# Optimization experiments

Hardware: AMD Instinct MI355X
Metric: run time of the kernel (lower is better)

Reference implementation:

```python
import jax, jax.numpy as jnp
import numpy as np

B = 16
CLS_OUT = 80
SCORE_THR = 0.05
IOU_THR = 0.65
MAX_NUM = 100
# FPN levels for a 1280x1280 input: (H, W, stride)
LEVELS = [(160, 160, 8), (80, 80, 16), (40, 40, 32)]
N = sum(h * w for h, w, _ in LEVELS)  # 33600


def make_priors():
    # mmdet MlvlPointGenerator(with_stride=True, offset=0): [x*stride, y*stride, stride, stride]
    ps = []
    for h, w, s in LEVELS:
        ys, xs = np.meshgrid(np.arange(h, dtype=np.float32), np.arange(w, dtype=np.float32), indexing='ij')
        st = np.full((h, w), float(s), dtype=np.float32)
        ps.append(np.stack([xs * s, ys * s, st, st], -1).reshape(-1, 4))
    return jnp.asarray(np.concatenate(ps, 0))


def setup_inputs() -> dict:
    key = jax.random.key(0)
    k1, k2, k3 = jax.random.split(key, 3)
    return {
        'cls_scores': jax.random.normal(k1, (B, N, CLS_OUT), dtype=jnp.float32),
        'bbox_preds': jax.random.normal(k2, (B, N, 4), dtype=jnp.float32),
        'objectness': jax.random.normal(k3, (B, N), dtype=jnp.float32),
        'priors': make_priors(),  # [N, 4]
    }


def _bbox_decode(priors, bbox_preds):
    # xy = pred_xy * stride + center;  wh = exp(pred_wh) * stride
    xys = bbox_preds[..., :2] * priors[:, 2:] + priors[:, :2]
    whs = jnp.exp(bbox_preds[..., 2:]) * priors[:, 2:]
    tl = xys - whs * 0.5
    br = xys + whs * 0.5
    return jnp.concatenate([tl, br], axis=-1)  # [B, N, 4] as (x1, y1, x2, y2)


def _iou_matrix(b1, b2):
    # b1: [M,4], b2: [M,4] -> [M,M], matching torch_cal_bbox_ious (no +1 offsets, eps=1e-8)
    x1 = jnp.maximum(b1[:, None, 0], b2[None, :, 0])
    y1 = jnp.maximum(b1[:, None, 1], b2[None, :, 1])
    x2 = jnp.minimum(b1[:, None, 2], b2[None, :, 2])
    y2 = jnp.minimum(b1[:, None, 3], b2[None, :, 3])
    inter = jnp.clip(x2 - x1, 0.0) * jnp.clip(y2 - y1, 0.0)
    a1 = (b1[:, 2] - b1[:, 0]) * (b1[:, 3] - b1[:, 1])
    a2 = (b2[:, 2] - b2[:, 0]) * (b2[:, 3] - b2[:, 1])
    union = a1[:, None] + a2[None, :] - inter
    return inter / (union + 1e-8)


def _nms_single(boxes, scores, labels, valid):
    # Take top MAX_NUM by score (invalid -> -inf), then class-aware greedy suppression.
    masked = jnp.where(valid, scores, -jnp.inf)
    order = jnp.argsort(-masked)[:MAX_NUM]
    b = boxes[order]          # [M,4]
    s = scores[order]         # [M]
    l = labels[order]         # [M]
    v = valid[order]          # [M]
    iou = _iou_matrix(b, b)
    same = l[:, None] == l[None, :]
    idx = jnp.arange(MAX_NUM)

    def body(i, keep):
        sup = keep[i] & same[i] & (iou[i] >= IOU_THR) & (idx > i)
        return keep & ~sup

    keep = jax.lax.fori_loop(0, MAX_NUM, body, v)
    dets = jnp.where(keep[:, None], jnp.concatenate([b, s[:, None]], -1), 0.0)  # [M,5]
    labs = jnp.where(keep, l, -1)
    return dets, labs, keep


def reference(cls_scores, bbox_preds, objectness, priors):
    cls = jax.nn.sigmoid(cls_scores)                  # [B,N,C]
    obj = jax.nn.sigmoid(objectness)                  # [B,N]
    bboxes = _bbox_decode(priors, bbox_preds)         # [B,N,4]
    max_scores = jnp.max(cls, axis=-1)                # [B,N]
    labels = jnp.argmax(cls, axis=-1).astype(jnp.int32)
    scores = max_scores * obj
    valid = scores >= SCORE_THR
    dets, labs, keep = jax.vmap(_nms_single)(bboxes, scores, labels, valid)
    out = jnp.concatenate([dets, labs[..., None].astype(jnp.float32)], -1)  # [B,MAX_NUM,6]
    return out, keep
```

## Files before the change

kernel.cpp:

```cpp
#include <hip/hip_runtime.h>
#include <cstddef>
#include <cstdint>

#define BB 16
#define NN 33600
#define CC 80
#define MAXN 100
#define NBINS 4096
#define MAXC 1024
#define SCORE_THR_F 0.05f
#define IOU_THR_F 0.65f

#define NCHUNK 525
#define K1_CPB 4
#define K1_GX ((NCHUNK + K1_CPB - 1) / K1_CPB)
#define K2T 512

__global__ __launch_bounds__(256) void k1_score(const float* __restrict__ cls,
                                                const float* __restrict__ obj,
                                                float* __restrict__ masked) {
  const int b = blockIdx.y;
  const int q = threadIdx.x & 3;
  const int r = threadIdx.x >> 2;
  const int c_end = min(blockIdx.x * K1_CPB + K1_CPB, NCHUNK);
  for (int c = blockIdx.x * K1_CPB; c < c_end; c++) {
    const int n = c * 64 + r;
    const float4* row = (const float4*)(cls + ((size_t)b * NN + n) * CC);
    float m = -INFINITY;
#pragma unroll
    for (int j = 0; j < 5; j++) {
      float4 v = row[q + 4 * j];
      m = fmaxf(m, fmaxf(fmaxf(v.x, v.y), fmaxf(v.z, v.w)));
    }
#pragma unroll
    for (int d = 1; d < 4; d <<= 1) m = fmaxf(m, __shfl_xor(m, d, 4));
    if (q == 0) {
      float o = obj[(size_t)b * NN + n];
      float s = (1.0f / (1.0f + expf(-m))) * (1.0f / (1.0f + expf(-o)));
      masked[(size_t)b * NN + n] = (s >= SCORE_THR_F) ? s : -INFINITY;
    }
  }
}

__device__ __forceinline__ int score_bin(float s) {
  return min(NBINS - 1, (int)(s * (float)NBINS));
}

__global__ __launch_bounds__(K2T) void k2_all(const float* __restrict__ cls,
                                              const float* __restrict__ bbox,
                                              const float* __restrict__ priors,
                                              const float* __restrict__ masked,
                                              float* __restrict__ out) {
  const int b = blockIdx.x;
  const int tid = threadIdx.x;

  __shared__ int hist[NBINS];
  __shared__ int sfx[K2T];
  __shared__ int s_t, s_cnt;
  __shared__ float cs[MAXC];
  __shared__ int ci[MAXC];
  __shared__ int sel[MAXN];
  __shared__ float sb[MAXN][4];
  __shared__ float ssc[MAXN];
  __shared__ int slab[MAXN];
  __shared__ unsigned int sup[MAXN][4];
  __shared__ unsigned int keepw[4];

  const float4* msc4 = (const float4*)(masked + (size_t)b * NN);

  for (int i = tid; i < NBINS; i += K2T) hist[i] = 0;
  if (tid == 0) { s_t = 0; s_cnt = 0; }
  __syncthreads();

  for (int i = tid; i < NN / 4; i += K2T) {
    float4 v = msc4[i];
    if (v.x >= SCORE_THR_F) atomicAdd(&hist[score_bin(v.x)], 1);
    if (v.y >= SCORE_THR_F) atomicAdd(&hist[score_bin(v.y)], 1);
    if (v.z >= SCORE_THR_F) atomicAdd(&hist[score_bin(v.z)], 1);
    if (v.w >= SCORE_THR_F) atomicAdd(&hist[score_bin(v.w)], 1);
  }
  __syncthreads();

  int sum = 0;
#pragma unroll
  for (int j = 0; j < NBINS / K2T; j++) sum += hist[tid * (NBINS / K2T) + j];
  sfx[tid] = sum;
  __syncthreads();
  for (int off = 1; off < K2T; off <<= 1) {
    int v = sfx[tid];
    int add = (tid + off < K2T) ? sfx[tid + off] : 0;
    __syncthreads();
    sfx[tid] = v + add;
    __syncthreads();
  }
  {
    int Sc = sfx[tid];
    int Sn = (tid < K2T - 1) ? sfx[tid + 1] : 0;
    if (Sc >= MAXN && Sn < MAXN) {
      int running = Sn;
      const int lo = tid * (NBINS / K2T);
      for (int bin = lo + (NBINS / K2T) - 1; bin >= lo; bin--) {
        running += hist[bin];
        if (running >= MAXN) { s_t = bin; break; }
      }
    }
  }
  __syncthreads();
  const int t = s_t;

  for (int i = tid; i < NN / 4; i += K2T) {
    float4 v = msc4[i];
    int base = i * 4;
    if (v.x >= SCORE_THR_F && score_bin(v.x) >= t) {
      int p = atomicAdd(&s_cnt, 1); if (p < MAXC) { cs[p] = v.x; ci[p] = base; }
    }
    if (v.y >= SCORE_THR_F && score_bin(v.y) >= t) {
      int p = atomicAdd(&s_cnt, 1); if (p < MAXC) { cs[p] = v.y; ci[p] = base + 1; }
    }
    if (v.z >= SCORE_THR_F && score_bin(v.z) >= t) {
      int p = atomicAdd(&s_cnt, 1); if (p < MAXC) { cs[p] = v.z; ci[p] = base + 2; }
    }
    if (v.w >= SCORE_THR_F && score_bin(v.w) >= t) {
      int p = atomicAdd(&s_cnt, 1); if (p < MAXC) { cs[p] = v.w; ci[p] = base + 3; }
    }
  }
  __syncthreads();
  const int C = min(s_cnt, MAXC);

  for (int k = tid; k < MAXN; k += K2T) sel[k] = -1;
  __syncthreads();

  for (int i = tid; i < C; i += K2T) {
    float si = cs[i]; int ii = ci[i];
    int r = 0;
    for (int j = 0; j < C; j++) {
      float sj = cs[j]; int ij = ci[j];
      r += (sj > si) || (sj == si && ij < ii);
    }
    if (r < MAXN) { sel[r] = ii; ssc[r] = si; }
  }
  __syncthreads();

  if (tid < MAXN) {
    int idx = sel[tid];
    if (idx >= 0) {
      float4 p = ((const float4*)priors)[idx];
      float4 d = ((const float4*)bbox)[(size_t)b * NN + idx];
      float cx = d.x * p.z + p.x;
      float cy = d.y * p.w + p.y;
      float hw = expf(d.z) * p.z * 0.5f;
      float hh = expf(d.w) * p.w * 0.5f;
      sb[tid][0] = cx - hw; sb[tid][1] = cy - hh;
      sb[tid][2] = cx + hw; sb[tid][3] = cy + hh;
      const float4* crow = (const float4*)(cls + ((size_t)b * NN + idx) * CC);
      float m = -INFINITY; int lab = 0;
#pragma unroll 4
      for (int j = 0; j < CC / 4; j++) {
        float4 v = crow[j];
        int c0 = 4 * j;
        if (v.x > m) { m = v.x; lab = c0; }
        if (v.y > m) { m = v.y; lab = c0 + 1; }
        if (v.z > m) { m = v.z; lab = c0 + 2; }
        if (v.w > m) { m = v.w; lab = c0 + 3; }
      }
      slab[tid] = lab;
    } else {
      sb[tid][0] = 0.f; sb[tid][1] = 0.f; sb[tid][2] = 0.f; sb[tid][3] = 0.f;
      ssc[tid] = 0.f; slab[tid] = -1;
    }
  }
  for (int i = tid; i < MAXN * 4; i += K2T) ((unsigned int*)sup)[i] = 0;
  __syncthreads();

  for (int p = tid; p < MAXN * MAXN; p += K2T) {
    int i = p / MAXN, j = p % MAXN;
    if (j > i && sel[i] >= 0 && sel[j] >= 0 && slab[i] == slab[j]) {
      float xx1 = fmaxf(sb[i][0], sb[j][0]);
      float yy1 = fmaxf(sb[i][1], sb[j][1]);
      float xx2 = fminf(sb[i][2], sb[j][2]);
      float yy2 = fminf(sb[i][3], sb[j][3]);
      float inter = fmaxf(xx2 - xx1, 0.f) * fmaxf(yy2 - yy1, 0.f);
      float ai = (sb[i][2] - sb[i][0]) * (sb[i][3] - sb[i][1]);
      float aj = (sb[j][2] - sb[j][0]) * (sb[j][3] - sb[j][1]);
      float iou = inter / (ai + aj - inter + 1e-8f);
      if (iou >= IOU_THR_F) atomicOr(&sup[i][j >> 5], 1u << (j & 31));
    }
  }
  __syncthreads();

  if (tid == 0) {
    unsigned int kw0 = 0, kw1 = 0, kw2 = 0, kw3 = 0;
    for (int k = 0; k < MAXN; k++)
      if (sel[k] >= 0) {
        if (k < 32) kw0 |= 1u << k;
        else if (k < 64) kw1 |= 1u << (k - 32);
        else if (k < 96) kw2 |= 1u << (k - 64);
        else kw3 |= 1u << (k - 96);
      }
    for (int i = 0; i < MAXN; i++) {
      unsigned int bit = (i < 32) ? (kw0 >> i) : (i < 64) ? (kw1 >> (i - 32))
                        : (i < 96) ? (kw2 >> (i - 64)) : (kw3 >> (i - 96));
      if (bit & 1u) {
        kw0 &= ~sup[i][0]; kw1 &= ~sup[i][1];
        kw2 &= ~sup[i][2]; kw3 &= ~sup[i][3];
      }
    }
    keepw[0] = kw0; keepw[1] = kw1; keepw[2] = kw2; keepw[3] = kw3;
  }
  __syncthreads();

  if (tid < MAXN) {
    int k = tid;
    bool kp = (keepw[k >> 5] >> (k & 31)) & 1u;
    float* row = out + ((size_t)b * MAXN + k) * 6;
    if (kp) {
      row[0] = sb[k][0]; row[1] = sb[k][1]; row[2] = sb[k][2]; row[3] = sb[k][3];
      row[4] = ssc[k];   row[5] = (float)slab[k];
    } else {
      row[0] = 0.f; row[1] = 0.f; row[2] = 0.f; row[3] = 0.f;
      row[4] = 0.f; row[5] = -1.f;
    }
    out[(size_t)BB * MAXN * 6 + (size_t)b * MAXN + k] = kp ? 1.0f : 0.0f;
  }
}

extern "C" void kernel_launch(void* const* d_in, const int* in_sizes, int n_in,
                              void* d_out, int out_size, void* d_ws, size_t ws_size,
                              hipStream_t stream) {
  const float* cls    = (const float*)d_in[0];
  const float* bbox   = (const float*)d_in[1];
  const float* obj    = (const float*)d_in[2];
  const float* priors = (const float*)d_in[3];
  float* out = (float*)d_out;
  float* masked = (float*)d_ws;

  k1_score<<<dim3(K1_GX, BB), 256, 0, stream>>>(cls, obj, masked);
  k2_all<<<BB, K2T, 0, stream>>>(cls, bbox, priors, masked, out);
}
```

Baseline: 293.0 us.

## Build score histogram in scoring kernel and stage class tiles through LDS

Moves the per-batch score histogram construction from the single-block-per-batch selection kernel into the wide scoring kernel, using global atomics into a zeroed workspace buffer. This removes a full serial pass over the masked scores in the low-parallelism kernel. The scoring kernel also now stages each 64-row class tile into shared memory with contiguous loads before the row max reduction. It adds a zeroing launch and global atomic contention.

After: 293.2 us. Within noise of the previous version (+0.1%).

```diff
diff --git a/kernel.cpp b/kernel.cpp
--- a/kernel.cpp
+++ b/kernel.cpp
@@ -12,32 +12,57 @@
 #define IOU_THR_F 0.65f
 
 #define NCHUNK 525
-#define K1_CPB 4
-#define K1_GX ((NCHUNK + K1_CPB - 1) / K1_CPB)
+#define K1_TPB 4
+#define K1_GX ((NCHUNK + K1_TPB - 1) / K1_TPB)
+#define TILE_F4 (64 * CC / 4)
 #define K2T 512
+
+#define OFF_GHIST (BB * NN * 4)
+
+__global__ __launch_bounds__(256) void k0_zero(int* __restrict__ p) {
+  int i = blockIdx.x * 256 + threadIdx.x;
+  if (i < BB * NBINS) p[i] = 0;
+}
 
 __global__ __launch_bounds__(256) void k1_score(const float* __restrict__ cls,
                                                 const float* __restrict__ obj,
-                                                float* __restrict__ masked) {
+                                                float* __restrict__ masked,
+                                                int* __restrict__ ghist) {
   const int b = blockIdx.y;
-  const int q = threadIdx.x & 3;
-  const int r = threadIdx.x >> 2;
-  const int c_end = min(blockIdx.x * K1_CPB + K1_CPB, NCHUNK);
-  for (int c = blockIdx.x * K1_CPB; c < c_end; c++) {
-    const int n = c * 64 + r;
-    const float4* row = (const float4*)(cls + ((size_t)b * NN + n) * CC);
+  const int tid = threadIdx.x;
+  const int q = tid & 3;
+  const int r = tid >> 2;
+  __shared__ float4 st[TILE_F4];
+
+  for (int ti = 0; ti < K1_TPB; ti++) {
+    const int tile = blockIdx.x * K1_TPB + ti;
+    if (tile >= NCHUNK) break;
+    const int n0 = tile * 64;
+    const float4* src = (const float4*)(cls + ((size_t)b * NN + n0) * CC);
+    __syncthreads();
+#pragma unroll
+    for (int j = 0; j < 5; j++) st[j * 256 + tid] = src[j * 256 + tid];
+    __syncthreads();
+
+    const float* rowp = (const float*)st + r * CC;
     float m = -INFINITY;
 #pragma unroll
     for (int j = 0; j < 5; j++) {
-      float4 v = row[q + 4 * j];
+      float4 v = *(const float4*)(rowp + (q + 4 * j) * 4);
       m = fmaxf(m, fmaxf(fmaxf(v.x, v.y), fmaxf(v.z, v.w)));
     }
 #pragma unroll
     for (int d = 1; d < 4; d <<= 1) m = fmaxf(m, __shfl_xor(m, d, 4));
     if (q == 0) {
+      const int n = n0 + r;
       float o = obj[(size_t)b * NN + n];
       float s = (1.0f / (1.0f + expf(-m))) * (1.0f / (1.0f + expf(-o)));
-      masked[(size_t)b * NN + n] = (s >= SCORE_THR_F) ? s : -INFINITY;
+      bool valid = (s >= SCORE_THR_F);
+      masked[(size_t)b * NN + n] = valid ? s : -INFINITY;
+      if (valid) {
+        int bin = min(NBINS - 1, (int)(s * (float)NBINS));
+        atomicAdd(&ghist[b * NBINS + bin], 1);
+      }
     }
   }
 }
@@ -50,6 +75,7 @@
                                               const float* __restrict__ bbox,
                                               const float* __restrict__ priors,
                                               const float* __restrict__ masked,
+                                              const int* __restrict__ ghist,
                                               float* __restrict__ out) {
   const int b = blockIdx.x;
   const int tid = threadIdx.x;
@@ -68,17 +94,8 @@
 
   const float4* msc4 = (const float4*)(masked + (size_t)b * NN);
 
-  for (int i = tid; i < NBINS; i += K2T) hist[i] = 0;
+  for (int i = tid; i < NBINS; i += K2T) hist[i] = ghist[b * NBINS + i];
   if (tid == 0) { s_t = 0; s_cnt = 0; }
-  __syncthreads();
-
-  for (int i = tid; i < NN / 4; i += K2T) {
-    float4 v = msc4[i];
-    if (v.x >= SCORE_THR_F) atomicAdd(&hist[score_bin(v.x)], 1);
-    if (v.y >= SCORE_THR_F) atomicAdd(&hist[score_bin(v.y)], 1);
-    if (v.z >= SCORE_THR_F) atomicAdd(&hist[score_bin(v.z)], 1);
-    if (v.w >= SCORE_THR_F) atomicAdd(&hist[score_bin(v.w)], 1);
-  }
   __syncthreads();
 
   int sum = 0;
@@ -232,8 +249,12 @@
   const float* obj    = (const float*)d_in[2];
   const float* priors = (const float*)d_in[3];
   float* out = (float*)d_out;
-  float* masked = (float*)d_ws;
-
-  k1_score<<<dim3(K1_GX, BB), 256, 0, stream>>>(cls, obj, masked);
-  k2_all<<<BB, K2T, 0, stream>>>(cls, bbox, priors, masked, out);
-}
+
+  char* ws = (char*)d_ws;
+  float* masked = (float*)ws;
+  int* ghist = (int*)(ws + OFF_GHIST);
+
+  k0_zero<<<(BB * NBINS + 255) / 256, 256, 0, stream>>>(ghist);
+  k1_score<<<dim3(K1_GX, BB), 256, 0, stream>>>(cls, obj, masked, ghist);
+  k2_all<<<BB, K2T, 0, stream>>>(cls, bbox, priors, masked, ghist, out);
+}
```
